# Performance work log

Hardware: AMD Instinct MI355X
Metric: run time of the kernel (lower is better)

## Reference

```python
import jax, jax.numpy as jnp
import numpy as np

OUT = 7          # out_size
SCALE = 0.125    # spatial_scale (1/8, FPN P3)
SAMPLES = 2      # sample_num


def setup_inputs() -> dict:
    key = jax.random.key(0)
    k1, k2, k3, k4, k5, k6, k7, k8, k9 = jax.random.split(key, 9)
    B, C, H, W = 2, 256, 256, 256
    n = 1024
    features = jax.random.normal(k1, (B, C, H, W), jnp.float32)
    # rois: (batch_idx, cx, cy, w, h, theta) in IMAGE coordinates
    bidx = jax.random.randint(k2, (n,), 0, B).astype(jnp.float32)
    cx = jax.random.uniform(k3, (n,), jnp.float32, 0.0, W / SCALE)
    cy = jax.random.uniform(k4, (n,), jnp.float32, 0.0, H / SCALE)
    rw = jax.random.uniform(k5, (n,), jnp.float32, 16.0, 512.0)
    rh = jax.random.uniform(k6, (n,), jnp.float32, 16.0, 512.0)
    ang = jax.random.uniform(k7, (n,), jnp.float32, -np.pi, np.pi)
    rois = jnp.stack([bidx, cx, cy, rw, rh, ang], axis=1)
    ic = OUT * OUT * C  # 12544
    fc = 1024
    w1 = jax.random.normal(k8, (ic, fc), jnp.float32) * 0.01
    b1 = jnp.zeros((fc,), jnp.float32)
    w2 = jax.random.normal(k9, (fc, OUT * OUT), jnp.float32) * 0.01
    b2 = jnp.zeros((OUT * OUT,), jnp.float32)
    return {"features": features, "rois": rois, "w1": w1, "b1": b1, "w2": w2, "b2": b2}


def _roi_align_rotated(features, rois):
    B, C, H, W = features.shape
    n = rois.shape[0]
    bidx = rois[:, 0].astype(jnp.int32)
    cx = rois[:, 1] * SCALE
    cy = rois[:, 2] * SCALE
    rw = jnp.maximum(rois[:, 3] * SCALE, 1.0)
    rh = jnp.maximum(rois[:, 4] * SCALE, 1.0)
    theta = rois[:, 5]
    bin_w = rw / OUT
    bin_h = rh / OUT
    g = jnp.arange(OUT, dtype=features.dtype)
    s = (jnp.arange(SAMPLES, dtype=features.dtype) + 0.5) / SAMPLES
    # roi-local sample coordinates: [n, OUT, SAMPLES]
    yy = -rh[:, None, None] / 2 + (g[None, :, None] + s[None, None, :]) * bin_h[:, None, None]
    xx = -rw[:, None, None] / 2 + (g[None, :, None] + s[None, None, :]) * bin_w[:, None, None]
    # broadcast to [n, oh, ow, sy, sx]
    yy = yy[:, :, None, :, None]
    xx = xx[:, None, :, None, :]
    ct = jnp.cos(theta)[:, None, None, None, None]
    st = jnp.sin(theta)[:, None, None, None, None]
    xs = xx * ct - yy * st + cx[:, None, None, None, None]
    ys = xx * st + yy * ct + cy[:, None, None, None, None]
    shp = (n, OUT, OUT, SAMPLES, SAMPLES)
    xs = jnp.broadcast_to(xs, shp).reshape(n, -1)  # [n, P], P = OUT*OUT*S*S
    ys = jnp.broadcast_to(ys, shp).reshape(n, -1)
    valid = (ys > -1.0) & (ys < H) & (xs > -1.0) & (xs < W)
    ysc = jnp.clip(ys, 0.0, H - 1)
    xsc = jnp.clip(xs, 0.0, W - 1)
    yl = jnp.floor(ysc).astype(jnp.int32)
    xl = jnp.floor(xsc).astype(jnp.int32)
    yh = jnp.minimum(yl + 1, H - 1)
    xh = jnp.minimum(xl + 1, W - 1)
    ly = ysc - yl
    lx = xsc - xl
    hy = 1.0 - ly
    hx = 1.0 - lx
    be = jnp.broadcast_to(bidx[:, None], yl.shape)
    # bilinear gathers: each [n, P, C]
    v11 = features[be, :, yl, xl]
    v12 = features[be, :, yl, xh]
    v21 = features[be, :, yh, xl]
    v22 = features[be, :, yh, xh]
    val = ((hy * hx)[..., None] * v11 + (hy * lx)[..., None] * v12
           + (ly * hx)[..., None] * v21 + (ly * lx)[..., None] * v22)
    val = val * valid[..., None].astype(val.dtype)
    # average the SAMPLES*SAMPLES points per bin -> [n, OUT, OUT, C]
    val = val.reshape(n, OUT, OUT, SAMPLES * SAMPLES, C).mean(axis=3)
    return jnp.transpose(val, (0, 3, 1, 2))  # [n, C, OUT, OUT]


def reference(features, rois, w1, b1, w2, b2):
    n = rois.shape[0]
    x = _roi_align_rotated(features, rois)          # [n, C, OUT, OUT]
    flat = x.reshape(n, -1)                          # [n, C*OUT*OUT]
    hid = jax.nn.relu(flat @ w1 + b1)
    mask = jax.nn.sigmoid(hid @ w2 + b2).reshape(n, 1, OUT, OUT)
    return x * mask
```

## Files before the change

kernel.cpp:

```cpp
#include <hip/hip_runtime.h>
#include <hip/hip_bf16.h>

typedef unsigned short u16;
typedef unsigned int u32;
typedef short short8 __attribute__((ext_vector_type(8)));
typedef float f32x4 __attribute__((ext_vector_type(4)));

#define OUTD 7
#define NROI 1024
#define CH 256
#define KDIM 12544
#define NHID 1024
#define KSPLIT 8

__device__ __forceinline__ float bf_lo(u32 u) {
    union { u32 i; float f; } v; v.i = u << 16; return v.f;
}
__device__ __forceinline__ float bf_hi(u32 u) {
    union { u32 i; float f; } v; v.i = u & 0xffff0000u; return v.f;
}
__device__ __forceinline__ u16 f2b(float f) {
    return (u16)(__bfloat16_as_ushort(__float2bfloat16(f)));
}
__device__ __forceinline__ void async16(const void* g, void* l) {
    __builtin_amdgcn_global_load_lds((const __attribute__((address_space(1))) u32*)g,
                                     (__attribute__((address_space(3))) u32*)l, 16, 0, 0);
}

__global__ __launch_bounds__(256) void transpose_feat(const float* __restrict__ f,
                                                      u16* __restrict__ ft) {
    __shared__ float tile[32][129];
    int pb = blockIdx.x;
    int cb = blockIdx.y;
    int b  = blockIdx.z;
    int tid = threadIdx.x;
    const float* src = f + ((size_t)(b * CH + cb * 32)) * 65536 + (size_t)pb * 128;
#pragma unroll
    for (int i = 0; i < 4; ++i) {
        int id = tid + 256 * i;
        int c = id >> 5, f4 = id & 31;
        float4 v = *(const float4*)(src + (size_t)c * 65536 + f4 * 4);
        tile[c][f4 * 4 + 0] = v.x;
        tile[c][f4 * 4 + 1] = v.y;
        tile[c][f4 * 4 + 2] = v.z;
        tile[c][f4 * 4 + 3] = v.w;
    }
    __syncthreads();
    u16* dst = ft + ((size_t)(b * 65536 + pb * 128)) * CH + cb * 32;
#pragma unroll
    for (int i = 0; i < 4; ++i) {
        int id = tid + 256 * i;
        int px = id >> 3, cg = id & 7;
        uint2 o;
        o.x = (u32)f2b(tile[cg * 4 + 0][px]) | ((u32)f2b(tile[cg * 4 + 1][px]) << 16);
        o.y = (u32)f2b(tile[cg * 4 + 2][px]) | ((u32)f2b(tile[cg * 4 + 3][px]) << 16);
        *(uint2*)(dst + (size_t)px * CH + cg * 4) = o;
    }
}

__global__ __launch_bounds__(256) void transpose_w1(const float* __restrict__ w1,
                                                    u16* __restrict__ w1t) {
    __shared__ float tile[32][129];
    int kb = blockIdx.x;
    int nb = blockIdx.y;
    int tid = threadIdx.x;
#pragma unroll
    for (int i = 0; i < 4; ++i) {
        int id = tid + 256 * i;
        int r = id >> 3, f4 = id & 7;
        float4 v = *(const float4*)(w1 + (size_t)(kb * 128 + r) * NHID + nb * 32 + f4 * 4);
        tile[f4 * 4 + 0][r] = v.x;
        tile[f4 * 4 + 1][r] = v.y;
        tile[f4 * 4 + 2][r] = v.z;
        tile[f4 * 4 + 3][r] = v.w;
    }
    __syncthreads();
#pragma unroll
    for (int i = 0; i < 4; ++i) {
        int id = tid + 256 * i;
        int nn = id >> 5, kg = id & 31;
        uint2 o;
        o.x = (u32)f2b(tile[nn][kg * 4 + 0]) | ((u32)f2b(tile[nn][kg * 4 + 1]) << 16);
        o.y = (u32)f2b(tile[nn][kg * 4 + 2]) | ((u32)f2b(tile[nn][kg * 4 + 3]) << 16);
        *(uint2*)(w1t + (size_t)(nb * 32 + nn) * KDIM + kb * 128 + kg * 4) = o;
    }
}

__global__ __launch_bounds__(256) void transpose_w2(const float* __restrict__ w2,
                                                    float* __restrict__ w2t) {
    int j = blockIdx.x;
    for (int k = threadIdx.x; k < NHID; k += 256)
        w2t[(size_t)j * NHID + k] = w2[(size_t)k * 49 + j];
}

__global__ __launch_bounds__(256) void roi_align(const u16* __restrict__ ft,
                                                 const float* __restrict__ rois,
                                                 u16* __restrict__ flat) {
    __shared__ u16 sbuf[49 * 260];
    int i = blockIdx.x;
    int tid = threadIdx.x;
    int lane = tid & 63, w = tid >> 6;
    float r0 = rois[i * 6 + 0], r1 = rois[i * 6 + 1], r2 = rois[i * 6 + 2];
    float r3 = rois[i * 6 + 3], r4 = rois[i * 6 + 4], th = rois[i * 6 + 5];
    int b = (int)r0;
    float cx = r1 * 0.125f, cy = r2 * 0.125f;
    float rw = fmaxf(r3 * 0.125f, 1.0f), rh = fmaxf(r4 * 0.125f, 1.0f);
    float bw = rw * (1.0f / 7.0f), bh = rh * (1.0f / 7.0f);
    float ct = cosf(th), st = sinf(th);
    const u16* fb = ft + (size_t)b * 65536 * CH;
    int coff = lane * 4;

    int start = w * 12 + (w > 0 ? 1 : 0);
    int cnt = (w == 0) ? 13 : 12;
    for (int bi = 0; bi < cnt; ++bi) {
        int bin = start + bi;
        int ph = bin / 7, pw = bin - ph * 7;
        float a0 = 0.f, a1 = 0.f, a2 = 0.f, a3 = 0.f;
#pragma unroll
        for (int s = 0; s < 4; ++s) {
            int sy = s >> 1, sx2 = s & 1;
            float yy = -rh * 0.5f + ((float)ph + ((float)sy + 0.5f) * 0.5f) * bh;
            float xx = -rw * 0.5f + ((float)pw + ((float)sx2 + 0.5f) * 0.5f) * bw;
            float xs = xx * ct - yy * st + cx;
            float ys = xx * st + yy * ct + cy;
            bool valid = (ys > -1.0f) && (ys < 256.0f) && (xs > -1.0f) && (xs < 256.0f);
            float ysc = fminf(fmaxf(ys, 0.f), 255.f);
            float xsc = fminf(fmaxf(xs, 0.f), 255.f);
            int yl = (int)floorf(ysc), xl = (int)floorf(xsc);
            int yh = min(yl + 1, 255), xh = min(xl + 1, 255);
            float ly = ysc - (float)yl, lx = xsc - (float)xl;
            float hy = 1.f - ly, hx = 1.f - lx;
            float w11 = hy * hx, w12 = hy * lx, w21 = ly * hx, w22 = ly * lx;
            if (!valid) { w11 = w12 = w21 = w22 = 0.f; }
            uint2 v11 = *(const uint2*)(fb + (((size_t)yl * 256 + xl) << 8) + coff);
            uint2 v12 = *(const uint2*)(fb + (((size_t)yl * 256 + xh) << 8) + coff);
            uint2 v21 = *(const uint2*)(fb + (((size_t)yh * 256 + xl) << 8) + coff);
            uint2 v22 = *(const uint2*)(fb + (((size_t)yh * 256 + xh) << 8) + coff);
            a0 += w11 * bf_lo(v11.x) + w12 * bf_lo(v12.x) + w21 * bf_lo(v21.x) + w22 * bf_lo(v22.x);
            a1 += w11 * bf_hi(v11.x) + w12 * bf_hi(v12.x) + w21 * bf_hi(v21.x) + w22 * bf_hi(v22.x);
            a2 += w11 * bf_lo(v11.y) + w12 * bf_lo(v12.y) + w21 * bf_lo(v21.y) + w22 * bf_lo(v22.y);
            a3 += w11 * bf_hi(v11.y) + w12 * bf_hi(v12.y) + w21 * bf_hi(v21.y) + w22 * bf_hi(v22.y);
        }
        uint2 o;
        o.x = (u32)f2b(a0 * 0.25f) | ((u32)f2b(a1 * 0.25f) << 16);
        o.y = (u32)f2b(a2 * 0.25f) | ((u32)f2b(a3 * 0.25f) << 16);
        *(uint2*)(sbuf + bin * 260 + coff) = o;
    }
    __syncthreads();
    uint2* fl = (uint2*)(flat + (size_t)i * KDIM);
#pragma unroll 1
    for (int k = tid; k < 3136; k += 256) {
        int e = k * 4;
        int c = e / 49, bn = e - c * 49;
        u16 r0_ = sbuf[bn * 260 + c]; if (++bn == 49) { bn = 0; ++c; }
        u16 r1_ = sbuf[bn * 260 + c]; if (++bn == 49) { bn = 0; ++c; }
        u16 r2_ = sbuf[bn * 260 + c]; if (++bn == 49) { bn = 0; ++c; }
        u16 r3_ = sbuf[bn * 260 + c];
        uint2 o;
        o.x = (u32)r0_ | ((u32)r1_ << 16);
        o.y = (u32)r2_ | ((u32)r3_ << 16);
        fl[k] = o;
    }
}

__global__ __launch_bounds__(256) void gemm1(const u16* __restrict__ A,
                                             const u16* __restrict__ Bt,
                                             float* __restrict__ part) {
    const int K = KDIM;
    int nb = blockIdx.x, mb = blockIdx.y, ks = blockIdx.z;
    int steps = 24 + (ks < 4 ? 1 : 0);
    int kbase = (ks * 24 + (ks < 4 ? ks : 4)) * 64;
    __shared__ u16 As[128 * 64];
    __shared__ u16 Bs[128 * 64];
    int tid = threadIdx.x;
    int lane = tid & 63, w = tid >> 6;
    int wm = w >> 1, wn = w & 1;
    f32x4 acc[4][4] = {};
    const u16* Ab = A + (size_t)(mb * 128) * K;
    const u16* Bb = Bt + (size_t)(nb * 128) * K;

    for (int s = 0; s < steps; ++s) {
        int kk = kbase + s * 64;
        __syncthreads();
#pragma unroll
        for (int j = 0; j < 4; ++j) {
            int c = w * 4 + j;
            int cid = c * 64 + lane;
            int row = cid >> 3, pq = cid & 7;
            int q = pq ^ (row & 7);
            async16(Ab + (size_t)row * K + kk + q * 8, As + c * 512 + lane * 8);
            async16(Bb + (size_t)row * K + kk + q * 8, Bs + c * 512 + lane * 8);
        }
        __syncthreads();
#pragma unroll
        for (int kh = 0; kh < 2; ++kh) {
            short8 af[4], bf[4];
#pragma unroll
            for (int t = 0; t < 4; ++t) {
                int q = kh * 4 + (lane >> 4);
                int r = wm * 64 + t * 16 + (lane & 15);
                int pq = q ^ (r & 7);
                af[t] = *(const short8*)(As + r * 64 + pq * 8);
                int rb = wn * 64 + t * 16 + (lane & 15);
                int pqb = q ^ (rb & 7);
                bf[t] = *(const short8*)(Bs + rb * 64 + pqb * 8);
            }
#pragma unroll
            for (int mt = 0; mt < 4; ++mt)
#pragma unroll
                for (int nt = 0; nt < 4; ++nt)
                    acc[mt][nt] = __builtin_amdgcn_mfma_f32_16x16x32_bf16(af[mt], bf[nt], acc[mt][nt], 0, 0, 0);
        }
    }
    float* P = part + (size_t)ks * NROI * NHID;
    int m_base = mb * 128 + wm * 64, n_base = nb * 128 + wn * 64;
#pragma unroll
    for (int mt = 0; mt < 4; ++mt)
#pragma unroll
        for (int nt = 0; nt < 4; ++nt)
#pragma unroll
            for (int i = 0; i < 4; ++i) {
                int m = m_base + mt * 16 + (lane >> 4) * 4 + i;
                int n = n_base + nt * 16 + (lane & 15);
                P[(size_t)m * NHID + n] = acc[mt][nt][i];
            }
}

__global__ __launch_bounds__(256) void reduce_relu(const float* __restrict__ part,
                                                   const float* __restrict__ b1,
                                                   float* __restrict__ hid) {
    int idx4 = blockIdx.x * 256 + threadIdx.x;
    const float4* pv = (const float4*)part;
    const float4* bv = (const float4*)b1;
    float4 s = bv[idx4 & 255];
#pragma unroll
    for (int j = 0; j < KSPLIT; ++j) {
        float4 p = pv[(size_t)j * 262144 + idx4];
        s.x += p.x; s.y += p.y; s.z += p.z; s.w += p.w;
    }
    float4 r;
    r.x = fmaxf(s.x, 0.f); r.y = fmaxf(s.y, 0.f);
    r.z = fmaxf(s.z, 0.f); r.w = fmaxf(s.w, 0.f);
    ((float4*)hid)[idx4] = r;
}

__global__ __launch_bounds__(256) void gemm2_apply(const float* __restrict__ hid,
                                                   const float* __restrict__ w2t,
                                                   const float* __restrict__ b2,
                                                   const u16* __restrict__ flat,
                                                   float* __restrict__ out) {
    __shared__ __align__(16) float hrow[NHID];
    __shared__ float partial[256];
    __shared__ float mrow[49];
    int i = blockIdx.x;
    int tid = threadIdx.x;
    for (int k = tid; k < NHID; k += 256) hrow[k] = hid[(size_t)i * NHID + k];
    __syncthreads();
    float p = 0.f;
    if (tid < 245) {
        int j = tid / 5, kc = tid - (tid / 5) * 5;
        int k0 = (256 * kc) / 5, k1 = (256 * (kc + 1)) / 5;
        const float4* wv = (const float4*)(w2t + (size_t)j * NHID);
        const float4* hv = (const float4*)hrow;
        for (int k = k0; k < k1; ++k) {
            float4 a = hv[k], b = wv[k];
            p += a.x * b.x + a.y * b.y + a.z * b.z + a.w * b.w;
        }
    }
    partial[tid] = p;
    __syncthreads();
    if (tid < 49) {
        float s = b2[tid];
#pragma unroll
        for (int q = 0; q < 5; ++q) s += partial[tid * 5 + q];
        mrow[tid] = 1.f / (1.f + expf(-s));
    }
    __syncthreads();
    const uint2* fl = (const uint2*)(flat + (size_t)i * KDIM);
    float4* op = (float4*)(out + (size_t)i * KDIM);
#pragma unroll 1
    for (int idx = tid; idx < 3136; idx += 256) {
        uint2 v = fl[idx];
        int e = idx * 4;
        int pp = e - (e / 49) * 49;
        float4 r;
        r.x = bf_lo(v.x) * mrow[pp]; if (++pp == 49) pp = 0;
        r.y = bf_hi(v.x) * mrow[pp]; if (++pp == 49) pp = 0;
        r.z = bf_lo(v.y) * mrow[pp]; if (++pp == 49) pp = 0;
        r.w = bf_hi(v.y) * mrow[pp];
        op[idx] = r;
    }
}

extern "C" void kernel_launch(void* const* d_in, const int* in_sizes, int n_in,
                              void* d_out, int out_size, void* d_ws, size_t ws_size,
                              hipStream_t stream) {
    const float* features = (const float*)d_in[0];
    const float* rois     = (const float*)d_in[1];
    const float* w1       = (const float*)d_in[2];
    const float* b1       = (const float*)d_in[3];
    const float* w2       = (const float*)d_in[4];
    const float* b2       = (const float*)d_in[5];
    float* out = (float*)d_out;
    char* ws = (char*)d_ws;

    u16* featT  = (u16*)(ws);
    u16* flat   = (u16*)(ws + 67108864);
    u16* w1t    = (u16*)(ws + 92798976);
    float* part = (float*)(ws + 118489088);
    float* hid  = (float*)(ws + 152043520);
    float* w2t  = (float*)(ws + 156237824);

    transpose_feat<<<dim3(512, 8, 2), 256, 0, stream>>>(features, featT);
    transpose_w1<<<dim3(98, 32), 256, 0, stream>>>(w1, w1t);
    transpose_w2<<<49, 256, 0, stream>>>(w2, w2t);
    roi_align<<<NROI, 256, 0, stream>>>(featT, rois, flat);
    gemm1<<<dim3(8, 8, KSPLIT), 256, 0, stream>>>(flat, w1t, part);
    reduce_relu<<<1024, 256, 0, stream>>>(part, b1, hid);
    gemm2_apply<<<NROI, 256, 0, stream>>>(hid, w2t, b2, flat, out);
}
```

Measured before the change: 389.7 us.

## Double-buffer gemm1 LDS loads, fuse split-K reduce into gemm2, retile feature transpose

```diff
diff --git a/kernel.cpp b/kernel.cpp
--- a/kernel.cpp
+++ b/kernel.cpp
@@ -29,31 +29,33 @@
 
 __global__ __launch_bounds__(256) void transpose_feat(const float* __restrict__ f,
                                                       u16* __restrict__ ft) {
-    __shared__ float tile[32][129];
+    __shared__ u32 tile[64 * 133];
     int pb = blockIdx.x;
-    int cb = blockIdx.y;
-    int b  = blockIdx.z;
-    int tid = threadIdx.x;
-    const float* src = f + ((size_t)(b * CH + cb * 32)) * 65536 + (size_t)pb * 128;
-#pragma unroll
-    for (int i = 0; i < 4; ++i) {
-        int id = tid + 256 * i;
-        int c = id >> 5, f4 = id & 31;
-        float4 v = *(const float4*)(src + (size_t)c * 65536 + f4 * 4);
-        tile[c][f4 * 4 + 0] = v.x;
-        tile[c][f4 * 4 + 1] = v.y;
-        tile[c][f4 * 4 + 2] = v.z;
-        tile[c][f4 * 4 + 3] = v.w;
-    }
-    __syncthreads();
-    u16* dst = ft + ((size_t)(b * 65536 + pb * 128)) * CH + cb * 32;
-#pragma unroll
-    for (int i = 0; i < 4; ++i) {
-        int id = tid + 256 * i;
-        int px = id >> 3, cg = id & 7;
+    int b  = blockIdx.y;
+    int tid = threadIdx.x;
+    const float* src = f + (size_t)b * CH * 65536 + (size_t)pb * 64;
+#pragma unroll
+    for (int it = 0; it < 8; ++it) {
+        int id = tid + 256 * it;
+        int f4 = id & 15, c2 = id >> 4;
+        const float* s0 = src + (size_t)(2 * c2) * 65536 + f4 * 4;
+        float4 a = *(const float4*)(s0);
+        float4 bb = *(const float4*)(s0 + 65536);
+#pragma unroll
+        for (int j = 0; j < 4; ++j) {
+            float av = (&a.x)[j], bv = (&bb.x)[j];
+            tile[(f4 * 4 + j) * 133 + c2] = (u32)f2b(av) | ((u32)f2b(bv) << 16);
+        }
+    }
+    __syncthreads();
+    u16* dst = ft + ((size_t)b * 65536 + (size_t)pb * 64) * CH;
+#pragma unroll
+    for (int it = 0; it < 16; ++it) {
+        int px = it * 4 + (tid >> 6);
+        int cg = tid & 63;
         uint2 o;
-        o.x = (u32)f2b(tile[cg * 4 + 0][px]) | ((u32)f2b(tile[cg * 4 + 1][px]) << 16);
-        o.y = (u32)f2b(tile[cg * 4 + 2][px]) | ((u32)f2b(tile[cg * 4 + 3][px]) << 16);
+        o.x = tile[px * 133 + cg * 2];
+        o.y = tile[px * 133 + cg * 2 + 1];
         *(uint2*)(dst + (size_t)px * CH + cg * 4) = o;
     }
 }
@@ -170,8 +172,8 @@
     int nb = blockIdx.x, mb = blockIdx.y, ks = blockIdx.z;
     int steps = 24 + (ks < 4 ? 1 : 0);
     int kbase = (ks * 24 + (ks < 4 ? ks : 4)) * 64;
-    __shared__ u16 As[128 * 64];
-    __shared__ u16 Bs[128 * 64];
+    __shared__ __align__(16) u16 As[2][128 * 64];
+    __shared__ __align__(16) u16 Bs[2][128 * 64];
     int tid = threadIdx.x;
     int lane = tid & 63, w = tid >> 6;
     int wm = w >> 1, wn = w & 1;
@@ -179,19 +181,30 @@
     const u16* Ab = A + (size_t)(mb * 128) * K;
     const u16* Bb = Bt + (size_t)(nb * 128) * K;
 
-    for (int s = 0; s < steps; ++s) {
-        int kk = kbase + s * 64;
-        __syncthreads();
+    auto stage = [&](int buf, int kk) {
 #pragma unroll
         for (int j = 0; j < 4; ++j) {
             int c = w * 4 + j;
             int cid = c * 64 + lane;
             int row = cid >> 3, pq = cid & 7;
             int q = pq ^ (row & 7);
-            async16(Ab + (size_t)row * K + kk + q * 8, As + c * 512 + lane * 8);
-            async16(Bb + (size_t)row * K + kk + q * 8, Bs + c * 512 + lane * 8);
-        }
-        __syncthreads();
+            async16(Ab + (size_t)row * K + kk + q * 8, &As[buf][c * 512 + lane * 8]);
+            async16(Bb + (size_t)row * K + kk + q * 8, &Bs[buf][c * 512 + lane * 8]);
+        }
+    };
+
+    stage(0, kbase);
+    int cur = 0;
+    for (int s = 0; s < steps; ++s) {
+        if (s + 1 < steps) {
+            stage(cur ^ 1, kbase + (s + 1) * 64);
+            asm volatile("s_waitcnt vmcnt(8)" ::: "memory");
+        } else {
+            asm volatile("s_waitcnt vmcnt(0)" ::: "memory");
+        }
+        __builtin_amdgcn_s_barrier();
+        const u16* Asb = &As[cur][0];
+        const u16* Bsb = &Bs[cur][0];
 #pragma unroll
         for (int kh = 0; kh < 2; ++kh) {
             short8 af[4], bf[4];
@@ -200,10 +213,10 @@
                 int q = kh * 4 + (lane >> 4);
                 int r = wm * 64 + t * 16 + (lane & 15);
                 int pq = q ^ (r & 7);
-                af[t] = *(const short8*)(As + r * 64 + pq * 8);
+                af[t] = *(const short8*)(Asb + r * 64 + pq * 8);
                 int rb = wn * 64 + t * 16 + (lane & 15);
                 int pqb = q ^ (rb & 7);
-                bf[t] = *(const short8*)(Bs + rb * 64 + pqb * 8);
+                bf[t] = *(const short8*)(Bsb + rb * 64 + pqb * 8);
             }
 #pragma unroll
             for (int mt = 0; mt < 4; ++mt)
@@ -211,6 +224,8 @@
                 for (int nt = 0; nt < 4; ++nt)
                     acc[mt][nt] = __builtin_amdgcn_mfma_f32_16x16x32_bf16(af[mt], bf[nt], acc[mt][nt], 0, 0, 0);
         }
+        __builtin_amdgcn_s_barrier();
+        cur ^= 1;
     }
     float* P = part + (size_t)ks * NROI * NHID;
     int m_base = mb * 128 + wm * 64, n_base = nb * 128 + wn * 64;
@@ -226,25 +241,8 @@
             }
 }
 
-__global__ __launch_bounds__(256) void reduce_relu(const float* __restrict__ part,
+__global__ __launch_bounds__(256) void gemm2_apply(const float* __restrict__ part,
                                                    const float* __restrict__ b1,
-                                                   float* __restrict__ hid) {
-    int idx4 = blockIdx.x * 256 + threadIdx.x;
-    const float4* pv = (const float4*)part;
-    const float4* bv = (const float4*)b1;
-    float4 s = bv[idx4 & 255];
-#pragma unroll
-    for (int j = 0; j < KSPLIT; ++j) {
-        float4 p = pv[(size_t)j * 262144 + idx4];
-        s.x += p.x; s.y += p.y; s.z += p.z; s.w += p.w;
-    }
-    float4 r;
-    r.x = fmaxf(s.x, 0.f); r.y = fmaxf(s.y, 0.f);
-    r.z = fmaxf(s.z, 0.f); r.w = fmaxf(s.w, 0.f);
-    ((float4*)hid)[idx4] = r;
-}
-
-__global__ __launch_bounds__(256) void gemm2_apply(const float* __restrict__ hid,
                                                    const float* __restrict__ w2t,
                                                    const float* __restrict__ b2,
                                                    const u16* __restrict__ flat,
@@ -254,7 +252,19 @@
     __shared__ float mrow[49];
     int i = blockIdx.x;
     int tid = threadIdx.x;
-    for (int k = tid; k < NHID; k += 256) hrow[k] = hid[(size_t)i * NHID + k];
+    {
+        float4 s = ((const float4*)b1)[tid];
+        size_t base = (size_t)i * 256 + tid;
+#pragma unroll
+        for (int j = 0; j < KSPLIT; ++j) {
+            float4 p = ((const float4*)part)[(size_t)j * 262144 + base];
+            s.x += p.x; s.y += p.y; s.z += p.z; s.w += p.w;
+        }
+        float4 r;
+        r.x = fmaxf(s.x, 0.f); r.y = fmaxf(s.y, 0.f);
+        r.z = fmaxf(s.z, 0.f); r.w = fmaxf(s.w, 0.f);
+        ((float4*)hrow)[tid] = r;
+    }
     __syncthreads();
     float p = 0.f;
     if (tid < 245) {
@@ -308,14 +318,12 @@
     u16* flat   = (u16*)(ws + 67108864);
     u16* w1t    = (u16*)(ws + 92798976);
     float* part = (float*)(ws + 118489088);
-    float* hid  = (float*)(ws + 152043520);
-    float* w2t  = (float*)(ws + 156237824);
-
-    transpose_feat<<<dim3(512, 8, 2), 256, 0, stream>>>(features, featT);
+    float* w2t  = (float*)(ws + 152043520);
+
+    transpose_feat<<<dim3(1024, 2), 256, 0, stream>>>(features, featT);
     transpose_w1<<<dim3(98, 32), 256, 0, stream>>>(w1, w1t);
     transpose_w2<<<49, 256, 0, stream>>>(w2, w2t);
     roi_align<<<NROI, 256, 0, stream>>>(featT, rois, flat);
     gemm1<<<dim3(8, 8, KSPLIT), 256, 0, stream>>>(flat, w1t, part);
-    reduce_relu<<<1024, 256, 0, stream>>>(part, b1, hid);
-    gemm2_apply<<<NROI, 256, 0, stream>>>(hid, w2t, b2, flat, out);
-}
+    gemm2_apply<<<NROI, 256, 0, stream>>>(part, b1, w2t, b2, flat, out);
+}
```

Result: no change. 387.4 us (-0.6%).
